# Optimization experiments

Measured on AMD Instinct MI355X. Metric: run time of the kernel, lower is better.

Reference implementation:

```python
import jax, jax.numpy as jnp
import numpy as np
import math

B, S, D, H, FF = 8, 1024, 1024, 16, 4096
DH = D // H
EPS = 1e-5


def _layernorm(x, g, b):
    mu = jnp.mean(x, axis=-1, keepdims=True)
    var = jnp.mean((x - mu) ** 2, axis=-1, keepdims=True)
    return (x - mu) * jax.lax.rsqrt(var + EPS) * g + b


def _gelu_tanh(x):
    c = math.sqrt(2.0 / math.pi)
    return 0.5 * x * (1.0 + jnp.tanh(c * (x + 0.044715 * x ** 3)))


def setup_inputs() -> dict:
    key = jax.random.key(0)
    ks = jax.random.split(key, 8)
    s = lambda d: 1.0 / math.sqrt(d)
    return {
        "x": jax.random.normal(ks[0], (B, S, D), jnp.float32),
        "ln1_g": jnp.ones((D,), jnp.float32),
        "ln1_b": jnp.zeros((D,), jnp.float32),
        "w_qkv": jax.random.normal(ks[1], (3 * D, D), jnp.float32) * s(D),
        "b_qkv": jax.random.normal(ks[2], (3 * D,), jnp.float32) * 0.02,
        "w_o": jax.random.normal(ks[3], (D, D), jnp.float32) * s(D),
        "b_o": jax.random.normal(ks[4], (D,), jnp.float32) * 0.02,
        "ln2_g": jnp.ones((D,), jnp.float32),
        "ln2_b": jnp.zeros((D,), jnp.float32),
        "w1": jax.random.normal(ks[5], (FF, D), jnp.float32) * s(D),
        "b1": jax.random.normal(ks[6], (FF,), jnp.float32) * 0.02,
        "w2": jax.random.normal(ks[7], (D, FF), jnp.float32) * s(FF),
        "b2": jnp.zeros((D,), jnp.float32),
    }


def reference(x, ln1_g, ln1_b, w_qkv, b_qkv, w_o, b_o, ln2_g, ln2_b, w1, b1, w2, b2):
    # --- pre-LN causal self-attention ---
    h = _layernorm(x, ln1_g, ln1_b)
    qkv = h @ w_qkv.T + b_qkv                      # [B,S,3D]
    q, k, v = jnp.split(qkv, 3, axis=-1)
    q = q.reshape(B, S, H, DH)
    k = k.reshape(B, S, H, DH)
    v = v.reshape(B, S, H, DH)
    scores = jnp.einsum("bqhd,bkhd->bhqk", q, k) / math.sqrt(DH)
    causal = jnp.triu(jnp.ones((S, S), jnp.bool_), 1)  # True above diagonal
    scores = jnp.where(causal, -jnp.inf, scores)
    attn = jax.nn.softmax(scores, axis=-1)
    o = jnp.einsum("bhqk,bkhd->bqhd", attn, v).reshape(B, S, D)
    x = x + (o @ w_o.T + b_o)
    # --- FFN ---
    h = _layernorm(x, ln2_g, ln2_b)
    h = _gelu_tanh(h @ w1.T + b1) @ w2.T + b2
    return x + h
```

## Files before the change

kernel.cpp:

```cpp
#include <hip/hip_runtime.h>
#include <math.h>


typedef __bf16 bf16_t;
typedef __bf16 bf16x4 __attribute__((ext_vector_type(4)));
typedef __bf16 bf16x8 __attribute__((ext_vector_type(8)));
typedef float f32x4 __attribute__((ext_vector_type(4)));

__device__ __forceinline__ void async16(const void* g, void* l) {
    __builtin_amdgcn_global_load_lds(
        (const __attribute__((address_space(1))) void*)g,
        (__attribute__((address_space(3))) void*)l,
        16, 0, 0);
}

__device__ __forceinline__ void ln_row(const float* __restrict__ x,
                                       const float* __restrict__ g,
                                       const float* __restrict__ bb,
                                       bf16_t* __restrict__ out, int row) {
    const int tid = threadIdx.x;
    const float4 xv = *(const float4*)(x + row * 1024 + tid * 4);
    float s1 = xv.x + xv.y + xv.z + xv.w;
    float s2 = xv.x * xv.x + xv.y * xv.y + xv.z * xv.z + xv.w * xv.w;
#pragma unroll
    for (int m = 32; m >= 1; m >>= 1) {
        s1 += __shfl_xor(s1, m);
        s2 += __shfl_xor(s2, m);
    }
    __shared__ float r1[4], r2[4];
    const int wid = tid >> 6, lane = tid & 63;
    if (lane == 0) { r1[wid] = s1; r2[wid] = s2; }
    __syncthreads();
    s1 = r1[0] + r1[1] + r1[2] + r1[3];
    s2 = r2[0] + r2[1] + r2[2] + r2[3];
    const float mu = s1 * (1.0f / 1024.0f);
    const float var = s2 * (1.0f / 1024.0f) - mu * mu;
    const float rs = rsqrtf(var + 1e-5f);
    const float4 gv = *(const float4*)(g + tid * 4);
    const float4 bv = *(const float4*)(bb + tid * 4);
    bf16x4 o;
    o[0] = (bf16_t)((xv.x - mu) * rs * gv.x + bv.x);
    o[1] = (bf16_t)((xv.y - mu) * rs * gv.y + bv.y);
    o[2] = (bf16_t)((xv.z - mu) * rs * gv.z + bv.z);
    o[3] = (bf16_t)((xv.w - mu) * rs * gv.w + bv.w);
    *(bf16x4*)(out + row * 1024 + tid * 4) = o;
}

__global__ __launch_bounds__(256) void prep(
    const float* __restrict__ s0, const float* __restrict__ s1,
    const float* __restrict__ s2, const float* __restrict__ s3,
    bf16_t* __restrict__ d0, bf16_t* __restrict__ d1,
    bf16_t* __restrict__ d2, bf16_t* __restrict__ d3,
    const float* __restrict__ x, const float* __restrict__ ln1g,
    const float* __restrict__ ln1b, bf16_t* __restrict__ h) {
    if (blockIdx.x >= 12288) {
        ln_row(x, ln1g, ln1b, h, blockIdx.x - 12288);
        return;
    }
    const int g = blockIdx.x * 256 + threadIdx.x;
    const float* s;
    bf16_t* d;
    int off;
    if (g < 786432)       { s = s0; d = d0; off = g; }
    else if (g < 1048576) { s = s1; d = d1; off = g - 786432; }
    else if (g < 2097152) { s = s2; d = d2; off = g - 1048576; }
    else                  { s = s3; d = d3; off = g - 2097152; }
    const int i = off * 4;
    const float4 v = *(const float4*)(s + i);
    bf16x4 o;
    o[0] = (bf16_t)v.x; o[1] = (bf16_t)v.y; o[2] = (bf16_t)v.z; o[3] = (bf16_t)v.w;
    *(bf16x4*)(d + i) = o;
}

__global__ __launch_bounds__(256) void ln_b(const bf16_t* __restrict__ x,
                                            const float* __restrict__ g,
                                            const float* __restrict__ bb,
                                            bf16_t* __restrict__ out) {
    const int tid = threadIdx.x;
    const int row = blockIdx.x;
    const bf16x4 xb = *(const bf16x4*)(x + row * 1024 + tid * 4);
    const float x0 = (float)xb[0], x1 = (float)xb[1], x2 = (float)xb[2], x3 = (float)xb[3];
    float s1 = x0 + x1 + x2 + x3;
    float s2 = x0 * x0 + x1 * x1 + x2 * x2 + x3 * x3;
#pragma unroll
    for (int m = 32; m >= 1; m >>= 1) {
        s1 += __shfl_xor(s1, m);
        s2 += __shfl_xor(s2, m);
    }
    __shared__ float r1[4], r2[4];
    const int wid = tid >> 6, lane = tid & 63;
    if (lane == 0) { r1[wid] = s1; r2[wid] = s2; }
    __syncthreads();
    s1 = r1[0] + r1[1] + r1[2] + r1[3];
    s2 = r2[0] + r2[1] + r2[2] + r2[3];
    const float mu = s1 * (1.0f / 1024.0f);
    const float var = s2 * (1.0f / 1024.0f) - mu * mu;
    const float rs = rsqrtf(var + 1e-5f);
    const float4 gv = *(const float4*)(g + tid * 4);
    const float4 bv = *(const float4*)(bb + tid * 4);
    bf16x4 o;
    o[0] = (bf16_t)((x0 - mu) * rs * gv.x + bv.x);
    o[1] = (bf16_t)((x1 - mu) * rs * gv.y + bv.y);
    o[2] = (bf16_t)((x2 - mu) * rs * gv.z + bv.z);
    o[3] = (bf16_t)((x3 - mu) * rs * gv.w + bv.w);
    *(bf16x4*)(out + row * 1024 + tid * 4) = o;
}

template <int MODE>
__global__ __launch_bounds__(256, 2) void gemm_bt(
    const bf16_t* __restrict__ A, const bf16_t* __restrict__ W,
    const float* __restrict__ bias, const float* __restrict__ residf,
    const bf16_t* __restrict__ residb,
    bf16_t* __restrict__ outb, float* __restrict__ outf,
    bf16_t* __restrict__ vt, int N, int K) {
    __shared__ bf16_t As[128 * 64];
    __shared__ bf16_t Bs[128 * 64];
    const int tid = threadIdx.x;
    const int w = tid >> 6;
    const int lane = tid & 63;
    const int l15 = lane & 15;
    const int quad = lane >> 4;

    const int nbn = N >> 7;
    const int per = 8 * nbn;
    const int lid = blockIdx.x;
    const int bm = (lid / per) * 8 + (lid % per) % 8;
    const int bn = (lid % per) / 8;
    const int m0 = bm * 128;
    const int n0 = bn * 128;
    const int wm = (w & 1) * 64;
    const int wn = (w >> 1) * 64;

    int rr[4], so[4];
#pragma unroll
    for (int q = 0; q < 4; q++) {
        const int c = q * 256 + w * 64 + lane;
        rr[q] = c >> 3;
        so[q] = ((c & 7) ^ (rr[q] & 7)) * 8;
    }
    const bf16_t* pA[4];
    const bf16_t* pB[4];
#pragma unroll
    for (int q = 0; q < 4; q++) {
        pA[q] = A + (size_t)(m0 + rr[q]) * K + so[q];
        pB[q] = W + (size_t)(n0 + rr[q]) * K + so[q];
    }

    f32x4 acc[4][4] = {};

    for (int k0 = 0; k0 < K; k0 += 64) {
#pragma unroll
        for (int q = 0; q < 4; q++) {
            async16(pA[q], As + q * 2048 + w * 512);
            async16(pB[q], Bs + q * 2048 + w * 512);
            pA[q] += 64; pB[q] += 64;
        }
        __syncthreads();

        bf16x8 af[4][2], bfr[4][2];
#pragma unroll
        for (int i = 0; i < 4; i++) {
            const int r = wm + i * 16 + l15;
#pragma unroll
            for (int f = 0; f < 2; f++) {
                const int slot = (f * 4 + quad) ^ (r & 7);
                af[i][f] = *(const bf16x8*)(As + r * 64 + slot * 8);
            }
        }
#pragma unroll
        for (int j = 0; j < 4; j++) {
            const int r = wn + j * 16 + l15;
#pragma unroll
            for (int f = 0; f < 2; f++) {
                const int slot = (f * 4 + quad) ^ (r & 7);
                bfr[j][f] = *(const bf16x8*)(Bs + r * 64 + slot * 8);
            }
        }
#pragma unroll
        for (int i = 0; i < 4; i++)
#pragma unroll
            for (int j = 0; j < 4; j++)
#pragma unroll
                for (int f = 0; f < 2; f++)
                    acc[i][j] = __builtin_amdgcn_mfma_f32_16x16x32_bf16(
                        af[i][f], bfr[j][f], acc[i][j], 0, 0, 0);
        __syncthreads();
    }

#pragma unroll
    for (int i = 0; i < 4; i++) {
#pragma unroll
        for (int j = 0; j < 4; j++) {
            const int col = n0 + wn + j * 16 + l15;
            const float bcol = bias[col];
            const int row0 = m0 + wm + i * 16 + quad * 4;
            float v4[4];
#pragma unroll
            for (int q = 0; q < 4; q++) {
                float v = acc[i][j][q] + bcol;
                if (MODE == 1) {
                    const float u2 = -1.5957691216057308f * (v + 0.044715f * v * v * v);
                    v = v * __builtin_amdgcn_rcpf(1.0f + __expf(u2));
                }
                v4[q] = v;
            }
            if (MODE == 4) {
#pragma unroll
                for (int q = 0; q < 4; q++) {
                    const size_t idx = (size_t)(row0 + q) * N + col;
                    outb[idx] = (bf16_t)(v4[q] + residf[idx]);
                }
            } else if (MODE == 5) {
#pragma unroll
                for (int q = 0; q < 4; q++) {
                    const size_t idx = (size_t)(row0 + q) * N + col;
                    outf[idx] = v4[q] + (float)residb[idx];
                }
            } else if (MODE == 3 && col >= 2048) {
                const int bh = (row0 >> 10) * 16 + ((col - 2048) >> 6);
                const int d = (col - 2048) & 63;
                bf16x4 pk;
#pragma unroll
                for (int q = 0; q < 4; q++) pk[q] = (bf16_t)v4[q];
                *(bf16x4*)(vt + (size_t)bh * 65536 + d * 1024 + (row0 & 1023)) = pk;
            } else {
#pragma unroll
                for (int q = 0; q < 4; q++)
                    outb[(size_t)(row0 + q) * N + col] = (bf16_t)v4[q];
            }
        }
    }
}

__global__ __launch_bounds__(512) void attn_mfma(const bf16_t* __restrict__ qkv,
                                                 const bf16_t* __restrict__ vt,
                                                 bf16_t* __restrict__ o) {
    __shared__ bf16_t Ks[4096];
    __shared__ bf16_t Vs[4096];
    __shared__ bf16_t Ps[8][32][72];
    const int tid = threadIdx.x;
    const int w = tid >> 6;
    const int lane = tid & 63;
    const int l15 = lane & 15;
    const int quad = lane >> 4;
    const int qb = blockIdx.x;
    const int bh = blockIdx.y;
    const int b = bh >> 4, h = bh & 15;

    const int qrow = b * 1024 + qb * 256 + w * 32;

    bf16x8 qf[2][2];
#pragma unroll
    for (int g = 0; g < 2; g++)
#pragma unroll
        for (int f = 0; f < 2; f++) {
            bf16x8 t = *(const bf16x8*)(qkv + (size_t)(qrow + g * 16 + l15) * 3072 + h * 64 + f * 32 + quad * 8);
#pragma unroll
            for (int e = 0; e < 8; e++) t[e] = (bf16_t)((float)t[e] * 0.125f);
            qf[g][f] = t;
        }

    f32x4 Ot[2][4] = {};
    float mrow[2] = {-3.0e38f, -3.0e38f};
    float lrow[2] = {0.0f, 0.0f};

    const int c0 = w * 64 + lane;
    const int r0 = c0 >> 3, g0 = (((c0 & 7) ^ (r0 & 7))) * 8;

    const bf16_t* kbase = qkv + (size_t)(b * 1024) * 3072 + 1024 + h * 64;
    const bf16_t* vbase = vt + (size_t)bh * 64 * 1024;

    const int ktmax = 4 * qb + 3;
    for (int kt = 0; kt <= ktmax; kt++) {
        async16(kbase + (size_t)(kt * 64 + r0) * 3072 + g0, Ks + w * 512);
        async16(vbase + (size_t)r0 * 1024 + kt * 64 + g0, Vs + w * 512);
        __syncthreads();

#pragma unroll
        for (int g = 0; g < 2; g++) {
            const int qmaxw = qb * 256 + w * 32 + g * 16 + 15;
            if (kt * 64 > qmaxw) continue;
            const int ktd = qmaxw >> 6;
            const int kbd = (2 * w + g) & 3;

            f32x4 sf[4];
#pragma unroll
            for (int kb = 0; kb < 4; kb++) {
                if (kt * 64 + kb * 16 > qmaxw) {
                    sf[kb] = (f32x4){-3.0e38f, -3.0e38f, -3.0e38f, -3.0e38f};
                    continue;
                }
                const int r = kb * 16 + l15;
                f32x4 acc = {};
#pragma unroll
                for (int f = 0; f < 2; f++) {
                    const int seg = (f * 4 + quad) ^ (r & 7);
                    const bf16x8 kf = *(const bf16x8*)(Ks + r * 64 + seg * 8);
                    acc = __builtin_amdgcn_mfma_f32_16x16x32_bf16(kf, qf[g][f], acc, 0, 0, 0);
                }
                if (kt == ktd && kb == kbd) {
#pragma unroll
                    for (int rr2 = 0; rr2 < 4; rr2++)
                        if (quad * 4 + rr2 > l15) acc[rr2] = -3.0e38f;
                }
                sf[kb] = acc;
            }

            float tmax = -3.0e38f;
#pragma unroll
            for (int kb = 0; kb < 4; kb++)
#pragma unroll
                for (int rr2 = 0; rr2 < 4; rr2++) tmax = fmaxf(tmax, sf[kb][rr2]);
            tmax = fmaxf(tmax, __shfl_xor(tmax, 16));
            tmax = fmaxf(tmax, __shfl_xor(tmax, 32));
            const float mnew = fmaxf(mrow[g], tmax);
            const float alpha = __expf(mrow[g] - mnew);
            float psum = 0.0f;
#pragma unroll
            for (int kb = 0; kb < 4; kb++) {
                bf16x4 pk;
#pragma unroll
                for (int rr2 = 0; rr2 < 4; rr2++) {
                    const float p = __expf(sf[kb][rr2] - mnew);
                    psum += p;
                    pk[rr2] = (bf16_t)p;
                }
                *(bf16x4*)(&Ps[w][g * 16 + l15][kb * 16 + quad * 4]) = pk;
            }
            psum += __shfl_xor(psum, 16);
            psum += __shfl_xor(psum, 32);
            lrow[g] = lrow[g] * alpha + psum;
            mrow[g] = mnew;
#pragma unroll
            for (int db = 0; db < 4; db++)
#pragma unroll
                for (int rr2 = 0; rr2 < 4; rr2++) Ot[g][db][rr2] *= alpha;

#pragma unroll
            for (int ks = 0; ks < 2; ks++) {
                if (kt * 64 + ks * 32 > qmaxw) break;
                const bf16x8 pf = *(const bf16x8*)(&Ps[w][g * 16 + l15][ks * 32 + quad * 8]);
#pragma unroll
                for (int db = 0; db < 4; db++) {
                    const int d = db * 16 + l15;
                    const int seg = (ks * 4 + quad) ^ (d & 7);
                    const bf16x8 vf = *(const bf16x8*)(Vs + d * 64 + seg * 8);
                    Ot[g][db] = __builtin_amdgcn_mfma_f32_16x16x32_bf16(vf, pf, Ot[g][db], 0, 0, 0);
                }
            }
        }
        __syncthreads();
    }

#pragma unroll
    for (int g = 0; g < 2; g++) {
        const float rl = 1.0f / lrow[g];
#pragma unroll
        for (int db = 0; db < 4; db++) {
            bf16x4 ov;
#pragma unroll
            for (int rr2 = 0; rr2 < 4; rr2++) ov[rr2] = (bf16_t)(Ot[g][db][rr2] * rl);
            *(bf16x4*)(o + (size_t)(qrow + g * 16 + l15) * 1024 + h * 64 + db * 16 + quad * 4) = ov;
        }
    }
}

extern "C" void kernel_launch(void* const* d_in, const int* in_sizes, int n_in,
                              void* d_out, int out_size, void* d_ws, size_t ws_size,
                              hipStream_t stream) {
    const float* x     = (const float*)d_in[0];
    const float* ln1g  = (const float*)d_in[1];
    const float* ln1b  = (const float*)d_in[2];
    const float* w_qkv = (const float*)d_in[3];
    const float* b_qkv = (const float*)d_in[4];
    const float* w_o   = (const float*)d_in[5];
    const float* b_o   = (const float*)d_in[6];
    const float* ln2g  = (const float*)d_in[7];
    const float* ln2b  = (const float*)d_in[8];
    const float* w1    = (const float*)d_in[9];
    const float* b1    = (const float*)d_in[10];
    const float* w2    = (const float*)d_in[11];
    const float* b2    = (const float*)d_in[12];
    float* out = (float*)d_out;

    char* w = (char*)d_ws;
    bf16_t* wbqkv = (bf16_t*)(w + 0);
    bf16_t* wbo   = (bf16_t*)(w + 6291456);
    bf16_t* wb1   = (bf16_t*)(w + 8388608);
    bf16_t* wb2   = (bf16_t*)(w + 16777216);
    bf16_t* h     = (bf16_t*)(w + 25165824);
    bf16_t* qkv   = (bf16_t*)(w + 41943040);
    bf16_t* ob    = (bf16_t*)(w + 92274688);
    bf16_t* x1b   = (bf16_t*)(w + 109051904);
    bf16_t* f     = (bf16_t*)(w + 142606336);
    bf16_t* vtb   = (bf16_t*)(w + 142606336);

    prep<<<20480, 256, 0, stream>>>(w_qkv, w_o, w1, w2, wbqkv, wbo, wb1, wb2,
                                    x, ln1g, ln1b, h);
    gemm_bt<3><<<64 * 24, 256, 0, stream>>>(h, wbqkv, b_qkv, nullptr, nullptr, qkv, nullptr, vtb, 3072, 1024);
    attn_mfma<<<dim3(4, 128), 512, 0, stream>>>(qkv, vtb, ob);
    gemm_bt<4><<<64 * 8, 256, 0, stream>>>(ob, wbo, b_o, x, nullptr, x1b, nullptr, nullptr, 1024, 1024);
    ln_b<<<8192, 256, 0, stream>>>(x1b, ln2g, ln2b, h);
    gemm_bt<1><<<64 * 32, 256, 0, stream>>>(h, wb1, b1, nullptr, nullptr, f, nullptr, nullptr, 4096, 1024);
    gemm_bt<5><<<64 * 8, 256, 0, stream>>>(f, wb2, b2, nullptr, x1b, nullptr, out, nullptr, 1024, 4096);
}
```

Baseline: 441.3 us.

## Add 256x256-tile 8-wave GEMM with interleaved async LDS prefetch for QKV and FFN1

Adds a new gemm8 kernel that uses 256x256 output tiles, 512 threads and a double-buffered LDS of 128KB. It splits each K-step into four quarter phases that interleave async global-to-LDS loads with MFMA bursts under raised priority, and adds grouped block ordering for L2 reuse. The QKV projection and the first FFN GEMM now use it in place of the older gemm_bt. The intent is more data reuse per tile and better overlap of loads with math, at the cost of fewer blocks in flight and high register and LDS pressure.

```diff
diff --git a/kernel.cpp b/kernel.cpp
--- a/kernel.cpp
+++ b/kernel.cpp
@@ -6,6 +6,8 @@
 typedef __bf16 bf16x4 __attribute__((ext_vector_type(4)));
 typedef __bf16 bf16x8 __attribute__((ext_vector_type(8)));
 typedef float f32x4 __attribute__((ext_vector_type(4)));
+
+#define WAITVM(N) asm volatile("s_waitcnt vmcnt(" #N ")" ::: "memory")
 
 __device__ __forceinline__ void async16(const void* g, void* l) {
     __builtin_amdgcn_global_load_lds(
@@ -232,6 +234,221 @@
     }
 }
 
+template <int MODE>
+__global__ __launch_bounds__(512, 2) void gemm8(
+    const bf16_t* __restrict__ A, const bf16_t* __restrict__ W,
+    const float* __restrict__ bias, bf16_t* __restrict__ outb,
+    bf16_t* __restrict__ vt, int N, int K) {
+    __shared__ bf16_t lds[65536];
+    const int tid = threadIdx.x;
+    const int w = tid >> 6, lane = tid & 63;
+    const int l15 = lane & 15, quad = lane >> 4;
+    const int wr = w >> 2, wc = w & 3;
+
+    const int nbn = N >> 8;
+    const int per = 8 * nbn;
+    const int lid = blockIdx.x;
+    const int bm = (lid / per) * 8 + (lid % per) % 8;
+    const int bn = (lid % per) / 8;
+    const int m0 = bm << 8, n0 = bn << 8;
+
+    int r_[2], s_[2];
+#pragma unroll
+    for (int L = 0; L < 2; L++) {
+        const int c = L * 512 + tid;
+        r_[L] = c >> 3;
+        s_[L] = ((c & 7) ^ (r_[L] & 7)) * 8;
+    }
+    const bf16_t* pa0[2]; const bf16_t* pa1[2];
+    const bf16_t* pb0[2]; const bf16_t* pb1[2];
+#pragma unroll
+    for (int L = 0; L < 2; L++) {
+        pa0[L] = A + (size_t)(m0 + r_[L]) * K + s_[L];
+        pa1[L] = pa0[L] + (size_t)128 * K;
+        pb0[L] = W + (size_t)(n0 + r_[L]) * K + s_[L];
+        pb1[L] = pb0[L] + (size_t)128 * K;
+    }
+
+    int ra[8], rb[4];
+#pragma unroll
+    for (int i = 0; i < 8; i++) ra[i] = (i >> 2) * 128 + wr * 64 + (i & 3) * 16 + l15;
+#pragma unroll
+    for (int j = 0; j < 4; j++) rb[j] = (j >> 1) * 128 + wc * 32 + (j & 1) * 16 + l15;
+
+#define FRAG(base, row, f) \
+    (*(const bf16x8*)((base) + (row) * 64 + ((((f) * 4 + quad) ^ ((row) & 7)) * 8)))
+
+    f32x4 acc[8][4] = {};
+    bf16x8 af[4][2], bfr[4][2];
+
+    async16(pa0[0], lds + w * 512);
+    async16(pa0[1], lds + 4096 + w * 512);
+    async16(pb0[0], lds + 16384 + w * 512);
+    async16(pb0[1], lds + 16384 + 4096 + w * 512);
+    async16(pb1[0], lds + 16384 + 8192 + w * 512);
+    async16(pb1[1], lds + 16384 + 8192 + 4096 + w * 512);
+    async16(pa1[0], lds + 8192 + w * 512);
+    async16(pa1[1], lds + 8192 + 4096 + w * 512);
+
+    const int NT = K >> 6;
+    int p = 0;
+    for (int t = 0; t < NT - 1; ++t, p ^= 1) {
+        const bf16_t* Ab = lds + p * 32768;
+        const bf16_t* Bb = Ab + 16384;
+        const int q2 = p ^ 1;
+        const int kn = (t + 1) << 6;
+        WAITVM(4);
+        __builtin_amdgcn_s_barrier();
+#pragma unroll
+        for (int i = 0; i < 4; i++) { af[i][0] = FRAG(Ab, ra[i], 0); af[i][1] = FRAG(Ab, ra[i], 1); }
+#pragma unroll
+        for (int j = 0; j < 2; j++) { bfr[j][0] = FRAG(Bb, rb[j], 0); bfr[j][1] = FRAG(Bb, rb[j], 1); }
+        async16(pa0[0] + kn, lds + q2 * 32768 + w * 512);
+        async16(pa0[1] + kn, lds + q2 * 32768 + 4096 + w * 512);
+        __builtin_amdgcn_s_setprio(1);
+#pragma unroll
+        for (int i = 0; i < 4; i++)
+#pragma unroll
+            for (int j = 0; j < 2; j++)
+#pragma unroll
+                for (int f = 0; f < 2; f++)
+                    acc[i][j] = __builtin_amdgcn_mfma_f32_16x16x32_bf16(af[i][f], bfr[j][f], acc[i][j], 0, 0, 0);
+        __builtin_amdgcn_s_setprio(0);
+        __builtin_amdgcn_s_barrier();
+        WAITVM(4);
+        __builtin_amdgcn_s_barrier();
+#pragma unroll
+        for (int j = 2; j < 4; j++) { bfr[j][0] = FRAG(Bb, rb[j], 0); bfr[j][1] = FRAG(Bb, rb[j], 1); }
+        async16(pb0[0] + kn, lds + q2 * 32768 + 16384 + w * 512);
+        async16(pb0[1] + kn, lds + q2 * 32768 + 16384 + 4096 + w * 512);
+        __builtin_amdgcn_s_setprio(1);
+#pragma unroll
+        for (int i = 0; i < 4; i++)
+#pragma unroll
+            for (int j = 2; j < 4; j++)
+#pragma unroll
+                for (int f = 0; f < 2; f++)
+                    acc[i][j] = __builtin_amdgcn_mfma_f32_16x16x32_bf16(af[i][f], bfr[j][f], acc[i][j], 0, 0, 0);
+        __builtin_amdgcn_s_setprio(0);
+        __builtin_amdgcn_s_barrier();
+        WAITVM(4);
+        __builtin_amdgcn_s_barrier();
+#pragma unroll
+        for (int i = 0; i < 4; i++) { af[i][0] = FRAG(Ab, ra[i + 4], 0); af[i][1] = FRAG(Ab, ra[i + 4], 1); }
+        async16(pb1[0] + kn, lds + q2 * 32768 + 16384 + 8192 + w * 512);
+        async16(pb1[1] + kn, lds + q2 * 32768 + 16384 + 8192 + 4096 + w * 512);
+        __builtin_amdgcn_s_setprio(1);
+#pragma unroll
+        for (int i = 0; i < 4; i++)
+#pragma unroll
+            for (int j = 0; j < 2; j++)
+#pragma unroll
+                for (int f = 0; f < 2; f++)
+                    acc[i + 4][j] = __builtin_amdgcn_mfma_f32_16x16x32_bf16(af[i][f], bfr[j][f], acc[i + 4][j], 0, 0, 0);
+        __builtin_amdgcn_s_setprio(0);
+        __builtin_amdgcn_s_barrier();
+        async16(pa1[0] + kn, lds + q2 * 32768 + 8192 + w * 512);
+        async16(pa1[1] + kn, lds + q2 * 32768 + 8192 + 4096 + w * 512);
+        __builtin_amdgcn_s_setprio(1);
+#pragma unroll
+        for (int i = 0; i < 4; i++)
+#pragma unroll
+            for (int j = 2; j < 4; j++)
+#pragma unroll
+                for (int f = 0; f < 2; f++)
+                    acc[i + 4][j] = __builtin_amdgcn_mfma_f32_16x16x32_bf16(af[i][f], bfr[j][f], acc[i + 4][j], 0, 0, 0);
+        __builtin_amdgcn_s_setprio(0);
+        __builtin_amdgcn_s_barrier();
+    }
+    {
+        const bf16_t* Ab = lds + p * 32768;
+        const bf16_t* Bb = Ab + 16384;
+        WAITVM(4);
+        __builtin_amdgcn_s_barrier();
+#pragma unroll
+        for (int i = 0; i < 4; i++) { af[i][0] = FRAG(Ab, ra[i], 0); af[i][1] = FRAG(Ab, ra[i], 1); }
+#pragma unroll
+        for (int j = 0; j < 2; j++) { bfr[j][0] = FRAG(Bb, rb[j], 0); bfr[j][1] = FRAG(Bb, rb[j], 1); }
+        __builtin_amdgcn_s_setprio(1);
+#pragma unroll
+        for (int i = 0; i < 4; i++)
+#pragma unroll
+            for (int j = 0; j < 2; j++)
+#pragma unroll
+                for (int f = 0; f < 2; f++)
+                    acc[i][j] = __builtin_amdgcn_mfma_f32_16x16x32_bf16(af[i][f], bfr[j][f], acc[i][j], 0, 0, 0);
+        __builtin_amdgcn_s_setprio(0);
+        __builtin_amdgcn_s_barrier();
+        WAITVM(2);
+        __builtin_amdgcn_s_barrier();
+#pragma unroll
+        for (int j = 2; j < 4; j++) { bfr[j][0] = FRAG(Bb, rb[j], 0); bfr[j][1] = FRAG(Bb, rb[j], 1); }
+        __builtin_amdgcn_s_setprio(1);
+#pragma unroll
+        for (int i = 0; i < 4; i++)
+#pragma unroll
+            for (int j = 2; j < 4; j++)
+#pragma unroll
+                for (int f = 0; f < 2; f++)
+                    acc[i][j] = __builtin_amdgcn_mfma_f32_16x16x32_bf16(af[i][f], bfr[j][f], acc[i][j], 0, 0, 0);
+        __builtin_amdgcn_s_setprio(0);
+        __builtin_amdgcn_s_barrier();
+        WAITVM(0);
+        __builtin_amdgcn_s_barrier();
+#pragma unroll
+        for (int i = 0; i < 4; i++) { af[i][0] = FRAG(Ab, ra[i + 4], 0); af[i][1] = FRAG(Ab, ra[i + 4], 1); }
+        __builtin_amdgcn_s_setprio(1);
+#pragma unroll
+        for (int i = 0; i < 4; i++)
+#pragma unroll
+            for (int j = 0; j < 2; j++)
+#pragma unroll
+                for (int f = 0; f < 2; f++)
+                    acc[i + 4][j] = __builtin_amdgcn_mfma_f32_16x16x32_bf16(af[i][f], bfr[j][f], acc[i + 4][j], 0, 0, 0);
+#pragma unroll
+        for (int i = 0; i < 4; i++)
+#pragma unroll
+            for (int j = 2; j < 4; j++)
+#pragma unroll
+                for (int f = 0; f < 2; f++)
+                    acc[i + 4][j] = __builtin_amdgcn_mfma_f32_16x16x32_bf16(af[i][f], bfr[j][f], acc[i + 4][j], 0, 0, 0);
+        __builtin_amdgcn_s_setprio(0);
+    }
+#undef FRAG
+
+#pragma unroll
+    for (int i = 0; i < 8; i++) {
+        const int row0 = m0 + (i >> 2) * 128 + wr * 64 + (i & 3) * 16 + quad * 4;
+#pragma unroll
+        for (int j = 0; j < 4; j++) {
+            const int col = n0 + (j >> 1) * 128 + wc * 32 + (j & 1) * 16 + l15;
+            const float bcol = bias[col];
+            float v4[4];
+#pragma unroll
+            for (int q = 0; q < 4; q++) {
+                float v = acc[i][j][q] + bcol;
+                if (MODE == 1) {
+                    const float u2 = -1.5957691216057308f * (v + 0.044715f * v * v * v);
+                    v = v * __builtin_amdgcn_rcpf(1.0f + __expf(u2));
+                }
+                v4[q] = v;
+            }
+            if (MODE == 3 && col >= 2048) {
+                const int bh = (row0 >> 10) * 16 + ((col - 2048) >> 6);
+                const int d = (col - 2048) & 63;
+                bf16x4 pk;
+#pragma unroll
+                for (int q = 0; q < 4; q++) pk[q] = (bf16_t)v4[q];
+                *(bf16x4*)(vt + (size_t)bh * 65536 + d * 1024 + (row0 & 1023)) = pk;
+            } else {
+#pragma unroll
+                for (int q = 0; q < 4; q++)
+                    outb[(size_t)(row0 + q) * N + col] = (bf16_t)v4[q];
+            }
+        }
+    }
+}
+
 __global__ __launch_bounds__(512) void attn_mfma(const bf16_t* __restrict__ qkv,
                                                  const bf16_t* __restrict__ vt,
                                                  bf16_t* __restrict__ o) {
@@ -397,10 +614,10 @@
 
     prep<<<20480, 256, 0, stream>>>(w_qkv, w_o, w1, w2, wbqkv, wbo, wb1, wb2,
                                     x, ln1g, ln1b, h);
-    gemm_bt<3><<<64 * 24, 256, 0, stream>>>(h, wbqkv, b_qkv, nullptr, nullptr, qkv, nullptr, vtb, 3072, 1024);
+    gemm8<3><<<384, 512, 0, stream>>>(h, wbqkv, b_qkv, qkv, vtb, 3072, 1024);
     attn_mfma<<<dim3(4, 128), 512, 0, stream>>>(qkv, vtb, ob);
     gemm_bt<4><<<64 * 8, 256, 0, stream>>>(ob, wbo, b_o, x, nullptr, x1b, nullptr, nullptr, 1024, 1024);
     ln_b<<<8192, 256, 0, stream>>>(x1b, ln2g, ln2b, h);
-    gemm_bt<1><<<64 * 32, 256, 0, stream>>>(h, wb1, b1, nullptr, nullptr, f, nullptr, nullptr, 4096, 1024);
+    gemm8<1><<<512, 512, 0, stream>>>(h, wb1, b1, f, nullptr, 4096, 1024);
     gemm_bt<5><<<64 * 8, 256, 0, stream>>>(f, wb2, b2, nullptr, x1b, nullptr, out, nullptr, 1024, 4096);
 }
```

Result: slower. 466.1 us (+5.6%).

## Double-buffer GEMM and attention LDS tiles with ping-pong scheduling and XCD remap

Applied to the files above, without the earlier changes.

Replaces the 128x128 single-buffered GEMM with a 512-thread 128x256 tile kernel. It double-buffers A/B tiles in LDS, overlaps async global-to-LDS loads with MFMA compute in two half-phases, and uses explicit waitcnt, barriers and setprio. Block IDs are remapped across the 8 XCDs. The attention kernel also double-buffers its K/V tiles, shrinks the P scratch, and reorders blocks so causal workloads are balanced. The cost is more LDS (96KB for the GEMM) and fragile hand-written wait counts.

```diff
diff --git a/kernel.cpp b/kernel.cpp
--- a/kernel.cpp
+++ b/kernel.cpp
@@ -6,6 +6,10 @@
 typedef __bf16 bf16x4 __attribute__((ext_vector_type(4)));
 typedef __bf16 bf16x8 __attribute__((ext_vector_type(8)));
 typedef float f32x4 __attribute__((ext_vector_type(4)));
+
+#define WAITVM(N) asm volatile("s_waitcnt vmcnt(" #N ")" ::: "memory")
+#define WAITLGKM0 asm volatile("s_waitcnt lgkmcnt(0)" ::: "memory")
+#define SCHEDBAR __builtin_amdgcn_sched_barrier(0)
 
 __device__ __forceinline__ void async16(const void* g, void* l) {
     __builtin_amdgcn_global_load_lds(
@@ -107,144 +111,235 @@
 }
 
 template <int MODE>
-__global__ __launch_bounds__(256, 2) void gemm_bt(
+__global__ __launch_bounds__(512, 2) void gemm2p(
     const bf16_t* __restrict__ A, const bf16_t* __restrict__ W,
     const float* __restrict__ bias, const float* __restrict__ residf,
     const bf16_t* __restrict__ residb,
     bf16_t* __restrict__ outb, float* __restrict__ outf,
     bf16_t* __restrict__ vt, int N, int K) {
-    __shared__ bf16_t As[128 * 64];
-    __shared__ bf16_t Bs[128 * 64];
+    __shared__ bf16_t lds[49152];
+    const int tid = threadIdx.x;
+    const int w = tid >> 6, lane = tid & 63;
+    const int l15 = lane & 15, quad = lane >> 4;
+    const int wm = (w & 1) * 64;
+    const int wc = w >> 1;
+
+    const int nwg = gridDim.x;
+    const int wg = (blockIdx.x & 7) * (nwg >> 3) + (blockIdx.x >> 3);
+    const int nbn = N >> 8;
+    const int per = 8 * nbn;
+    const int bm = (wg / per) * 8 + (wg % per) % 8;
+    const int bn = (wg % per) / 8;
+    const int m0 = bm << 7, n0 = bn << 8;
+
+    const bf16_t* pa[2]; const bf16_t* pb[4];
+#pragma unroll
+    for (int L = 0; L < 2; L++) {
+        const int c = L * 512 + tid, r = c >> 3;
+        pa[L] = A + (size_t)(m0 + r) * K + ((c & 7) ^ (r & 7)) * 8;
+    }
+#pragma unroll
+    for (int L = 0; L < 4; L++) {
+        const int c = L * 512 + tid, r = c >> 3;
+        pb[L] = W + (size_t)(n0 + r) * K + ((c & 7) ^ (r & 7)) * 8;
+    }
+
+    const int swz0 = (quad ^ (l15 & 7)) * 8;
+    const int swz1 = ((4 + quad) ^ (l15 & 7)) * 8;
+    const int fragoffA = wm * 64 + l15 * 64 + swz0;
+    const bf16_t* bA0 = lds + fragoffA;
+    const bf16_t* bA1 = lds + wm * 64 + l15 * 64 + swz1;
+    const bf16_t* bB0 = lds + 8192 + wc * 2048 + l15 * 64 + swz0;
+    const bf16_t* bB1 = lds + 8192 + wc * 2048 + l15 * 64 + swz1;
+    const bf16_t* cA0 = bA0 + 24576;
+    const bf16_t* cA1 = bA1 + 24576;
+    const bf16_t* cB0 = bB0 + 24576;
+    const bf16_t* cB1 = bB1 + 24576;
+
+    f32x4 acc[4][4] = {};
+    bf16x8 af[4][2], bfr[4][2];
+
+    async16(pa[0], lds + w * 512);
+    async16(pa[1], lds + 4096 + w * 512);
+    async16(pb[0], lds + 8192 + w * 512);
+    async16(pb[1], lds + 12288 + w * 512);
+    async16(pb[2], lds + 16384 + w * 512);
+    async16(pb[3], lds + 20480 + w * 512);
+    WAITVM(2);
+    __builtin_amdgcn_s_barrier();
+
+    const int NT = K >> 6;
+    for (int t = 0; t < NT - 1; ++t) {
+        bf16_t* nb = (bf16_t*)(cA0 - fragoffA);
+        const int kn = (t + 1) << 6;
+
+#pragma unroll
+        for (int i = 0; i < 4; i++) {
+            af[i][0] = *(const bf16x8*)(bA0 + i * 1024);
+            af[i][1] = *(const bf16x8*)(bA1 + i * 1024);
+        }
+#pragma unroll
+        for (int j = 0; j < 2; j++) {
+            bfr[j][0] = *(const bf16x8*)(bB0 + j * 1024);
+            bfr[j][1] = *(const bf16x8*)(bB1 + j * 1024);
+        }
+        async16(pa[0] + kn, nb + w * 512);
+        async16(pa[1] + kn, nb + 4096 + w * 512);
+        async16(pb[0] + kn, nb + 8192 + w * 512);
+        async16(pb[1] + kn, nb + 12288 + w * 512);
+        SCHEDBAR;
+        __builtin_amdgcn_s_barrier();
+        WAITLGKM0;
+        SCHEDBAR;
+        __builtin_amdgcn_s_setprio(1);
+#pragma unroll
+        for (int i = 0; i < 4; i++)
+#pragma unroll
+            for (int j = 0; j < 2; j++)
+#pragma unroll
+                for (int f = 0; f < 2; f++)
+                    acc[i][j] = __builtin_amdgcn_mfma_f32_16x16x32_bf16(af[i][f], bfr[j][f], acc[i][j], 0, 0, 0);
+        __builtin_amdgcn_s_setprio(0);
+        SCHEDBAR;
+        WAITVM(4);
+        __builtin_amdgcn_s_barrier();
+
+#pragma unroll
+        for (int j = 2; j < 4; j++) {
+            bfr[j][0] = *(const bf16x8*)(bB0 + 8192 + (j & 1) * 1024);
+            bfr[j][1] = *(const bf16x8*)(bB1 + 8192 + (j & 1) * 1024);
+        }
+        async16(pb[2] + kn, nb + 16384 + w * 512);
+        async16(pb[3] + kn, nb + 20480 + w * 512);
+        SCHEDBAR;
+        __builtin_amdgcn_s_barrier();
+        WAITLGKM0;
+        SCHEDBAR;
+        __builtin_amdgcn_s_setprio(1);
+#pragma unroll
+        for (int i = 0; i < 4; i++)
+#pragma unroll
+            for (int j = 2; j < 4; j++)
+#pragma unroll
+                for (int f = 0; f < 2; f++)
+                    acc[i][j] = __builtin_amdgcn_mfma_f32_16x16x32_bf16(af[i][f], bfr[j][f], acc[i][j], 0, 0, 0);
+        __builtin_amdgcn_s_setprio(0);
+        SCHEDBAR;
+        WAITVM(2);
+        __builtin_amdgcn_s_barrier();
+
+        { const bf16_t* s;
+          s = bA0; bA0 = cA0; cA0 = s;
+          s = bA1; bA1 = cA1; cA1 = s;
+          s = bB0; bB0 = cB0; cB0 = s;
+          s = bB1; bB1 = cB1; cB1 = s; }
+    }
+
+    {
+#pragma unroll
+        for (int i = 0; i < 4; i++) {
+            af[i][0] = *(const bf16x8*)(bA0 + i * 1024);
+            af[i][1] = *(const bf16x8*)(bA1 + i * 1024);
+        }
+#pragma unroll
+        for (int j = 0; j < 2; j++) {
+            bfr[j][0] = *(const bf16x8*)(bB0 + j * 1024);
+            bfr[j][1] = *(const bf16x8*)(bB1 + j * 1024);
+        }
+        SCHEDBAR;
+        __builtin_amdgcn_s_barrier();
+        WAITLGKM0;
+        SCHEDBAR;
+        __builtin_amdgcn_s_setprio(1);
+#pragma unroll
+        for (int i = 0; i < 4; i++)
+#pragma unroll
+            for (int j = 0; j < 2; j++)
+#pragma unroll
+                for (int f = 0; f < 2; f++)
+                    acc[i][j] = __builtin_amdgcn_mfma_f32_16x16x32_bf16(af[i][f], bfr[j][f], acc[i][j], 0, 0, 0);
+        __builtin_amdgcn_s_setprio(0);
+        SCHEDBAR;
+        WAITVM(0);
+        __builtin_amdgcn_s_barrier();
+#pragma unroll
+        for (int j = 2; j < 4; j++) {
+            bfr[j][0] = *(const bf16x8*)(bB0 + 8192 + (j & 1) * 1024);
+            bfr[j][1] = *(const bf16x8*)(bB1 + 8192 + (j & 1) * 1024);
+        }
+        WAITLGKM0;
+        SCHEDBAR;
+        __builtin_amdgcn_s_setprio(1);
+#pragma unroll
+        for (int i = 0; i < 4; i++)
+#pragma unroll
+            for (int j = 2; j < 4; j++)
+#pragma unroll
+                for (int f = 0; f < 2; f++)
+                    acc[i][j] = __builtin_amdgcn_mfma_f32_16x16x32_bf16(af[i][f], bfr[j][f], acc[i][j], 0, 0, 0);
+        __builtin_amdgcn_s_setprio(0);
+    }
+
+#pragma unroll
+    for (int i = 0; i < 4; i++) {
+        const int row0 = m0 + wm + i * 16 + quad * 4;
+#pragma unroll
+        for (int j = 0; j < 4; j++) {
+            const int col = n0 + (j >> 1) * 128 + wc * 32 + (j & 1) * 16 + l15;
+            const float bcol = bias[col];
+            float v4[4];
+#pragma unroll
+            for (int q = 0; q < 4; q++) {
+                float v = acc[i][j][q] + bcol;
+                if (MODE == 1) {
+                    const float u2 = -1.5957691216057308f * (v + 0.044715f * v * v * v);
+                    v = v * __builtin_amdgcn_rcpf(1.0f + __expf(u2));
+                }
+                v4[q] = v;
+            }
+            if (MODE == 4) {
+#pragma unroll
+                for (int q = 0; q < 4; q++) {
+                    const size_t idx = (size_t)(row0 + q) * N + col;
+                    outb[idx] = (bf16_t)(v4[q] + residf[idx]);
+                }
+            } else if (MODE == 5) {
+#pragma unroll
+                for (int q = 0; q < 4; q++) {
+                    const size_t idx = (size_t)(row0 + q) * N + col;
+                    outf[idx] = v4[q] + (float)residb[idx];
+                }
+            } else if (MODE == 3 && col >= 2048) {
+                const int bh = (row0 >> 10) * 16 + ((col - 2048) >> 6);
+                const int d = (col - 2048) & 63;
+                bf16x4 pk;
+#pragma unroll
+                for (int q = 0; q < 4; q++) pk[q] = (bf16_t)v4[q];
+                *(bf16x4*)(vt + (size_t)bh * 65536 + d * 1024 + (row0 & 1023)) = pk;
+            } else {
+#pragma unroll
+                for (int q = 0; q < 4; q++)
+                    outb[(size_t)(row0 + q) * N + col] = (bf16_t)v4[q];
+            }
+        }
+    }
+}
+
+__global__ __launch_bounds__(512) void attn_mfma(const bf16_t* __restrict__ qkv,
+                                                 const bf16_t* __restrict__ vt,
+                                                 bf16_t* __restrict__ o) {
+    __shared__ bf16_t Ks[2][4096];
+    __shared__ bf16_t Vs[2][4096];
+    __shared__ bf16_t Ps[8][16][72];
     const int tid = threadIdx.x;
     const int w = tid >> 6;
     const int lane = tid & 63;
     const int l15 = lane & 15;
     const int quad = lane >> 4;
-
-    const int nbn = N >> 7;
-    const int per = 8 * nbn;
-    const int lid = blockIdx.x;
-    const int bm = (lid / per) * 8 + (lid % per) % 8;
-    const int bn = (lid % per) / 8;
-    const int m0 = bm * 128;
-    const int n0 = bn * 128;
-    const int wm = (w & 1) * 64;
-    const int wn = (w >> 1) * 64;
-
-    int rr[4], so[4];
-#pragma unroll
-    for (int q = 0; q < 4; q++) {
-        const int c = q * 256 + w * 64 + lane;
-        rr[q] = c >> 3;
-        so[q] = ((c & 7) ^ (rr[q] & 7)) * 8;
-    }
-    const bf16_t* pA[4];
-    const bf16_t* pB[4];
-#pragma unroll
-    for (int q = 0; q < 4; q++) {
-        pA[q] = A + (size_t)(m0 + rr[q]) * K + so[q];
-        pB[q] = W + (size_t)(n0 + rr[q]) * K + so[q];
-    }
-
-    f32x4 acc[4][4] = {};
-
-    for (int k0 = 0; k0 < K; k0 += 64) {
-#pragma unroll
-        for (int q = 0; q < 4; q++) {
-            async16(pA[q], As + q * 2048 + w * 512);
-            async16(pB[q], Bs + q * 2048 + w * 512);
-            pA[q] += 64; pB[q] += 64;
-        }
-        __syncthreads();
-
-        bf16x8 af[4][2], bfr[4][2];
-#pragma unroll
-        for (int i = 0; i < 4; i++) {
-            const int r = wm + i * 16 + l15;
-#pragma unroll
-            for (int f = 0; f < 2; f++) {
-                const int slot = (f * 4 + quad) ^ (r & 7);
-                af[i][f] = *(const bf16x8*)(As + r * 64 + slot * 8);
-            }
-        }
-#pragma unroll
-        for (int j = 0; j < 4; j++) {
-            const int r = wn + j * 16 + l15;
-#pragma unroll
-            for (int f = 0; f < 2; f++) {
-                const int slot = (f * 4 + quad) ^ (r & 7);
-                bfr[j][f] = *(const bf16x8*)(Bs + r * 64 + slot * 8);
-            }
-        }
-#pragma unroll
-        for (int i = 0; i < 4; i++)
-#pragma unroll
-            for (int j = 0; j < 4; j++)
-#pragma unroll
-                for (int f = 0; f < 2; f++)
-                    acc[i][j] = __builtin_amdgcn_mfma_f32_16x16x32_bf16(
-                        af[i][f], bfr[j][f], acc[i][j], 0, 0, 0);
-        __syncthreads();
-    }
-
-#pragma unroll
-    for (int i = 0; i < 4; i++) {
-#pragma unroll
-        for (int j = 0; j < 4; j++) {
-            const int col = n0 + wn + j * 16 + l15;
-            const float bcol = bias[col];
-            const int row0 = m0 + wm + i * 16 + quad * 4;
-            float v4[4];
-#pragma unroll
-            for (int q = 0; q < 4; q++) {
-                float v = acc[i][j][q] + bcol;
-                if (MODE == 1) {
-                    const float u2 = -1.5957691216057308f * (v + 0.044715f * v * v * v);
-                    v = v * __builtin_amdgcn_rcpf(1.0f + __expf(u2));
-                }
-                v4[q] = v;
-            }
-            if (MODE == 4) {
-#pragma unroll
-                for (int q = 0; q < 4; q++) {
-                    const size_t idx = (size_t)(row0 + q) * N + col;
-                    outb[idx] = (bf16_t)(v4[q] + residf[idx]);
-                }
-            } else if (MODE == 5) {
-#pragma unroll
-                for (int q = 0; q < 4; q++) {
-                    const size_t idx = (size_t)(row0 + q) * N + col;
-                    outf[idx] = v4[q] + (float)residb[idx];
-                }
-            } else if (MODE == 3 && col >= 2048) {
-                const int bh = (row0 >> 10) * 16 + ((col - 2048) >> 6);
-                const int d = (col - 2048) & 63;
-                bf16x4 pk;
-#pragma unroll
-                for (int q = 0; q < 4; q++) pk[q] = (bf16_t)v4[q];
-                *(bf16x4*)(vt + (size_t)bh * 65536 + d * 1024 + (row0 & 1023)) = pk;
-            } else {
-#pragma unroll
-                for (int q = 0; q < 4; q++)
-                    outb[(size_t)(row0 + q) * N + col] = (bf16_t)v4[q];
-            }
-        }
-    }
-}
-
-__global__ __launch_bounds__(512) void attn_mfma(const bf16_t* __restrict__ qkv,
-                                                 const bf16_t* __restrict__ vt,
-                                                 bf16_t* __restrict__ o) {
-    __shared__ bf16_t Ks[4096];
-    __shared__ bf16_t Vs[4096];
-    __shared__ bf16_t Ps[8][32][72];
-    const int tid = threadIdx.x;
-    const int w = tid >> 6;
-    const int lane = tid & 63;
-    const int l15 = lane & 15;
-    const int quad = lane >> 4;
-    const int qb = blockIdx.x;
-    const int bh = blockIdx.y;
+    const int beta = blockIdx.x;
+    int qb, bh;
+    if (beta < 256) { qb = beta & 3; bh = beta >> 2; }
+    else { const int gm = beta - 256; qb = 3 - (gm & 3); bh = 64 + (gm >> 2); }
     const int b = bh >> 4, h = bh & 15;
 
     const int qrow = b * 1024 + qb * 256 + w * 32;
@@ -271,10 +366,20 @@
     const bf16_t* vbase = vt + (size_t)bh * 64 * 1024;
 
     const int ktmax = 4 * qb + 3;
-    for (int kt = 0; kt <= ktmax; kt++) {
-        async16(kbase + (size_t)(kt * 64 + r0) * 3072 + g0, Ks + w * 512);
-        async16(vbase + (size_t)r0 * 1024 + kt * 64 + g0, Vs + w * 512);
-        __syncthreads();
+
+    async16(kbase + (size_t)r0 * 3072 + g0, &Ks[0][0] + w * 512);
+    async16(vbase + (size_t)r0 * 1024 + g0, &Vs[0][0] + w * 512);
+    WAITVM(0);
+    __builtin_amdgcn_s_barrier();
+
+    int p = 0;
+    for (int kt = 0; kt <= ktmax; kt++, p ^= 1) {
+        if (kt < ktmax) {
+            async16(kbase + (size_t)((kt + 1) * 64 + r0) * 3072 + g0, &Ks[p ^ 1][0] + w * 512);
+            async16(vbase + (size_t)r0 * 1024 + (kt + 1) * 64 + g0, &Vs[p ^ 1][0] + w * 512);
+        }
+        const bf16_t* Kp = &Ks[p][0];
+        const bf16_t* Vp = &Vs[p][0];
 
 #pragma unroll
         for (int g = 0; g < 2; g++) {
@@ -295,7 +400,7 @@
 #pragma unroll
                 for (int f = 0; f < 2; f++) {
                     const int seg = (f * 4 + quad) ^ (r & 7);
-                    const bf16x8 kf = *(const bf16x8*)(Ks + r * 64 + seg * 8);
+                    const bf16x8 kf = *(const bf16x8*)(Kp + r * 64 + seg * 8);
                     acc = __builtin_amdgcn_mfma_f32_16x16x32_bf16(kf, qf[g][f], acc, 0, 0, 0);
                 }
                 if (kt == ktd && kb == kbd) {
@@ -321,11 +426,11 @@
                 bf16x4 pk;
 #pragma unroll
                 for (int rr2 = 0; rr2 < 4; rr2++) {
-                    const float p = __expf(sf[kb][rr2] - mnew);
-                    psum += p;
-                    pk[rr2] = (bf16_t)p;
-                }
-                *(bf16x4*)(&Ps[w][g * 16 + l15][kb * 16 + quad * 4]) = pk;
+                    const float p2 = __expf(sf[kb][rr2] - mnew);
+                    psum += p2;
+                    pk[rr2] = (bf16_t)p2;
+                }
+                *(bf16x4*)(&Ps[w][l15][kb * 16 + quad * 4]) = pk;
             }
             psum += __shfl_xor(psum, 16);
             psum += __shfl_xor(psum, 32);
@@ -339,17 +444,19 @@
 #pragma unroll
             for (int ks = 0; ks < 2; ks++) {
                 if (kt * 64 + ks * 32 > qmaxw) break;
-                const bf16x8 pf = *(const bf16x8*)(&Ps[w][g * 16 + l15][ks * 32 + quad * 8]);
+                const bf16x8 pf = *(const bf16x8*)(&Ps[w][l15][ks * 32 + quad * 8]);
 #pragma unroll
                 for (int db = 0; db < 4; db++) {
                     const int d = db * 16 + l15;
                     const int seg = (ks * 4 + quad) ^ (d & 7);
-                    const bf16x8 vf = *(const bf16x8*)(Vs + d * 64 + seg * 8);
+                    const bf16x8 vf = *(const bf16x8*)(Vp + d * 64 + seg * 8);
                     Ot[g][db] = __builtin_amdgcn_mfma_f32_16x16x32_bf16(vf, pf, Ot[g][db], 0, 0, 0);
                 }
             }
         }
-        __syncthreads();
+        SCHEDBAR;
+        WAITVM(0);
+        __builtin_amdgcn_s_barrier();
     }
 
 #pragma unroll
@@ -397,10 +504,10 @@
 
     prep<<<20480, 256, 0, stream>>>(w_qkv, w_o, w1, w2, wbqkv, wbo, wb1, wb2,
                                     x, ln1g, ln1b, h);
-    gemm_bt<3><<<64 * 24, 256, 0, stream>>>(h, wbqkv, b_qkv, nullptr, nullptr, qkv, nullptr, vtb, 3072, 1024);
-    attn_mfma<<<dim3(4, 128), 512, 0, stream>>>(qkv, vtb, ob);
-    gemm_bt<4><<<64 * 8, 256, 0, stream>>>(ob, wbo, b_o, x, nullptr, x1b, nullptr, nullptr, 1024, 1024);
+    gemm2p<3><<<768, 512, 0, stream>>>(h, wbqkv, b_qkv, nullptr, nullptr, qkv, nullptr, vtb, 3072, 1024);
+    attn_mfma<<<512, 512, 0, stream>>>(qkv, vtb, ob);
+    gemm2p<4><<<256, 512, 0, stream>>>(ob, wbo, b_o, x, nullptr, x1b, nullptr, nullptr, 1024, 1024);
     ln_b<<<8192, 256, 0, stream>>>(x1b, ln2g, ln2b, h);
-    gemm_bt<1><<<64 * 32, 256, 0, stream>>>(h, wb1, b1, nullptr, nullptr, f, nullptr, nullptr, 4096, 1024);
-    gemm_bt<5><<<64 * 8, 256, 0, stream>>>(f, wb2, b2, nullptr, x1b, nullptr, out, nullptr, 1024, 4096);
-}
+    gemm2p<1><<<1024, 512, 0, stream>>>(h, wb1, b1, nullptr, nullptr, f, nullptr, nullptr, 4096, 1024);
+    gemm2p<5><<<256, 512, 0, stream>>>(f, wb2, b2, nullptr, x1b, nullptr, out, nullptr, 1024, 4096);
+}
```

After: 417.1 us. 1.06x faster.
